# Kernel tuning notes

Measured on AMD Instinct MI355X. Metric: run time of the kernel, lower is better.

## Reference

```python
import jax, jax.numpy as jnp
import numpy as np

B, C, H, W = 16, 512, 64, 64
NH, HD = 8, 64  # num_heads, head_dim; C == NH*HD
EPS_ATTN = 1e-5
EPS_BN = 1e-5


def setup_inputs() -> dict:
    key = jax.random.key(0)
    k = jax.random.split(key, 9)
    x = jax.random.normal(k[0], (B, C, H, W), dtype=jnp.float32)
    # grouped 1x1 conv qkv: groups=NH, in/group=HD, out/group=3*HD
    w1 = jax.random.normal(k[1], (NH, 3 * HD, HD), dtype=jnp.float32) * 0.05
    b1 = jax.random.normal(k[2], (NH, 3 * HD), dtype=jnp.float32) * 0.01
    # grouped 1x1 conv qkv2: groups=HD, in/group=NH, out/group=3*NH
    w2 = jax.random.normal(k[3], (HD, 3 * NH, NH), dtype=jnp.float32) * 0.05
    b2 = jax.random.normal(k[4], (HD, 3 * NH), dtype=jnp.float32) * 0.01
    gamma = 1.0 + 0.1 * jax.random.normal(k[5], (C,), dtype=jnp.float32)
    beta = 0.1 * jax.random.normal(k[6], (C,), dtype=jnp.float32)
    rmean = 0.1 * jax.random.normal(k[7], (C,), dtype=jnp.float32)
    rvar = 0.5 + jax.random.uniform(k[8], (C,), dtype=jnp.float32)
    return {"x": x, "w1": w1, "b1": b1, "w2": w2, "b2": b2,
            "gamma": gamma, "beta": beta, "rmean": rmean, "rvar": rvar}


def _signed_sqrt_softmax(a):
    a = jnp.sign(a) * jnp.sqrt(jnp.abs(a) + EPS_ATTN)
    return jax.nn.softmax(a, axis=-1)


def reference(x, w1, b1, w2, b2, gamma, beta, rmean, rvar):
    N = H * W
    # ---- stage 1: grouped 1x1 conv (groups=NH) ----
    xg = x.reshape(B, NH, HD, N)
    qkv = jnp.einsum('goi,bgin->bgon', w1, xg) + b1[None, :, :, None]  # [B,NH,3HD,N]
    # torch grouped-conv channel order is group-major -> flatten then split as in source
    q, k, v = jnp.moveaxis(qkv.reshape(B, 3 * C, N).reshape(B, 3, NH, HD, N), 1, 0)
    attn = jnp.einsum('bhdn,bhen->bhde', q, k) * (HD ** -0.5)  # [B,NH,HD,HD]
    attn = _signed_sqrt_softmax(attn)
    out = jnp.einsum('bhde,bhen->bhdn', attn, v)  # [B,NH,HD,N]
    x1 = out.reshape(B, C, H, W) + x
    x1 = jnp.transpose(x1.reshape(B, NH, HD, H, W), (0, 2, 1, 3, 4)).reshape(B, C, H, W)
    # ---- BatchNorm2d (eval mode) + ReLU ----
    inv = gamma / jnp.sqrt(rvar + EPS_BN)
    y = x1 * inv[None, :, None, None] + (beta - rmean * inv)[None, :, None, None]
    xr = jnp.maximum(y, 0.0)
    # ---- stage 2: grouped 1x1 conv (groups=HD) ----
    xg2 = xr.reshape(B, HD, NH, N)
    qkv2 = jnp.einsum('goi,bgin->bgon', w2, xg2) + b2[None, :, :, None]  # [B,HD,3NH,N]
    q2, k2, v2 = jnp.moveaxis(qkv2.reshape(B, 3 * C, N).reshape(B, 3, HD, NH, N), 1, 0)
    attn2 = jnp.einsum('bdhn,bden->bdhe', q2, k2) * (NH ** -0.5)  # [B,HD,NH,NH]
    attn2 = _signed_sqrt_softmax(attn2)
    out2 = jnp.einsum('bdhe,bden->bdhn', attn2, v2)  # [B,HD,NH,N]
    x2 = jnp.transpose(out2.reshape(B, HD, NH, H, W), (0, 2, 1, 3, 4)).reshape(B, C, H, W) + y
    return x2
```

## Files before the change

kernel.cpp:

```cpp
#include <hip/hip_runtime.h>

#define N_ 4096

typedef __attribute__((ext_vector_type(8))) short bf16x8;
typedef __attribute__((ext_vector_type(4))) short bf16x4;
typedef __attribute__((ext_vector_type(4))) float f32x4;

__device__ __forceinline__ float ssqrt(float a) {
  if (a == 0.f) return 0.f;
  return copysignf(sqrtf(fabsf(a) + 1e-5f), a);
}

__device__ __forceinline__ ushort f2bf(float f) {
  uint u = __float_as_uint(f);
  u += 0x7fff + ((u >> 16) & 1);
  return (ushort)(u >> 16);
}
__device__ __forceinline__ float bf2f(ushort h) {
  return __uint_as_float((uint)h << 16);
}

__device__ __forceinline__ void split2(float f, ushort& hi, ushort& lo) {
  uint u = __float_as_uint(f);
  hi = (ushort)(u >> 16);
  float lof = f - __uint_as_float(u & 0xffff0000u);
  lo = (ushort)(__float_as_uint(lof) >> 16);
}

__device__ __forceinline__ f32x4 mfma16(bf16x8 a, bf16x8 b, f32x4 c) {
  return __builtin_amdgcn_mfma_f32_16x16x32_bf16(a, b, c, 0, 0, 0);
}

__device__ __forceinline__ bf16x8 relu8(bf16x8 v) {
  union { bf16x8 h; uint u[4]; } x;
  x.h = v;
#pragma unroll
  for (int i = 0; i < 4; ++i) {
    uint m = x.u[i] & 0x80008000u;
    x.u[i] &= ~((m >> 15) * 0xFFFFu);
  }
  return x.h;
}

__device__ __forceinline__ bf16x8 ld8_b64(const ushort* p) {
  bf16x4 a = *(const bf16x4*)p;
  bf16x4 b = *(const bf16x4*)(p + 4);
  return (bf16x8){a[0], a[1], a[2], a[3], b[0], b[1], b[2], b[3]};
}

__global__ __launch_bounds__(256) void k1_gram(const float* __restrict__ x,
    float* __restrict__ Gp, float* __restrict__ sums) {
  const int GQ[6] = {0, 0, 1, 1, 2, 2};
  const int GK[6] = {2, 3, 3, 4, 4, 5};
  int bid = (blockIdx.x & 7) * 48 + (blockIdx.x >> 3);
  int s = bid / 96, rem = bid % 96;
  int b = rem / 6, pid = rem % 6;
  int gq = GQ[pid], gk = GK[pid];
  const float* A = x + ((size_t)b * 512 + gq * 64) * N_ + s * 1024;
  const float* B = x + ((size_t)b * 512 + gk * 64) * N_ + s * 1024;
  __shared__ __attribute__((aligned(16))) ushort Ah[64][72], Al[64][72];
  __shared__ __attribute__((aligned(16))) ushort Bh[64][72], Bl[64][72];
  int t = threadIdx.x;
  int lr = t >> 2, lq = t & 3;
  int l = t & 63, w = t >> 6;
  int mw = (w >> 1) * 32, nw = (w & 1) * 32;
  int fr = l & 15, ko = (l >> 4) * 8;
  float sumA = 0.f, sumB = 0.f;
  f32x4 acc[2][2];
#pragma unroll
  for (int i = 0; i < 2; ++i)
#pragma unroll
    for (int j = 0; j < 2; ++j) acc[i][j] = (f32x4){0.f, 0.f, 0.f, 0.f};

  for (int kt = 0; kt < 16; ++kt) {
    int kbase = kt * 64 + lq * 16;
#pragma unroll
    for (int j = 0; j < 4; ++j) {
      float4 va = *(const float4*)(A + (size_t)lr * N_ + kbase + j * 4);
      float4 vb = *(const float4*)(B + (size_t)lr * N_ + kbase + j * 4);
      sumA += va.x + va.y + va.z + va.w;
      sumB += vb.x + vb.y + vb.z + vb.w;
      ushort4 ha, la, hb, lb;
      split2(va.x, ha.x, la.x); split2(va.y, ha.y, la.y);
      split2(va.z, ha.z, la.z); split2(va.w, ha.w, la.w);
      split2(vb.x, hb.x, lb.x); split2(vb.y, hb.y, lb.y);
      split2(vb.z, hb.z, lb.z); split2(vb.w, hb.w, lb.w);
      int c0 = lq * 16 + j * 4;
      *(ushort4*)&Ah[lr][c0] = ha;
      *(ushort4*)&Al[lr][c0] = la;
      *(ushort4*)&Bh[lr][c0] = hb;
      *(ushort4*)&Bl[lr][c0] = lb;
    }
    __syncthreads();
#pragma unroll
    for (int wk = 0; wk < 2; ++wk) {
      int kk = wk * 32 + ko;
      bf16x8 ah[2], al[2], bh[2], bl[2];
#pragma unroll
      for (int mt = 0; mt < 2; ++mt) {
        ah[mt] = *(const bf16x8*)&Ah[mw + mt * 16 + fr][kk];
        al[mt] = *(const bf16x8*)&Al[mw + mt * 16 + fr][kk];
      }
#pragma unroll
      for (int nt = 0; nt < 2; ++nt) {
        bh[nt] = *(const bf16x8*)&Bh[nw + nt * 16 + fr][kk];
        bl[nt] = *(const bf16x8*)&Bl[nw + nt * 16 + fr][kk];
      }
#pragma unroll
      for (int mt = 0; mt < 2; ++mt)
#pragma unroll
        for (int nt = 0; nt < 2; ++nt) {
          acc[mt][nt] = mfma16(ah[mt], bh[nt], acc[mt][nt]);
          acc[mt][nt] = mfma16(ah[mt], bl[nt], acc[mt][nt]);
          acc[mt][nt] = mfma16(al[mt], bh[nt], acc[mt][nt]);
        }
    }
    __syncthreads();
  }
  size_t base = ((size_t)s * 96 + rem) * 4096;
#pragma unroll
  for (int mt = 0; mt < 2; ++mt)
#pragma unroll
    for (int nt = 0; nt < 2; ++nt)
#pragma unroll
      for (int reg = 0; reg < 4; ++reg) {
        int gr = mw + mt * 16 + (l >> 4) * 4 + reg;
        int gc = nw + nt * 16 + fr;
        Gp[base + (size_t)gr * 64 + gc] = acc[mt][nt][reg];
      }
  sumA += __shfl_xor(sumA, 1); sumA += __shfl_xor(sumA, 2);
  sumB += __shfl_xor(sumB, 1); sumB += __shfl_xor(sumB, 2);
  if (lq == 0) {
    sums[(((size_t)s * 16 + b) * 6 + gq) * 64 + lr] = sumA;
    sums[(((size_t)s * 16 + b) * 6 + gk) * 64 + lr] = sumB;
  }
}

__global__ __launch_bounds__(256) void k2_attn1(
    const float* __restrict__ w1, const float* __restrict__ b1,
    const float* __restrict__ Gp, const float* __restrict__ sums,
    ushort* __restrict__ M1h, ushort* __restrict__ M1l,
    float* __restrict__ pbv1) {
  const int PID[8] = {0, 1, 1, 2, 3, 3, 4, 5};
  int bh = blockIdx.x;
  int b = bh >> 3, h = bh & 7;
  int pid = PID[h];
  int mq = h, mk = 8 + h, mv = 16 + h;
  int gq = mq / 3, oq0 = (mq % 3) * 64;
  int gk = mk / 3, ok0 = (mk % 3) * 64;
  int gv = mv / 3, ov0 = (mv % 3) * 64;
  __shared__ __attribute__((aligned(16))) float Gs[64][68];
  __shared__ __attribute__((aligned(16))) float Was[64][68];
  __shared__ __attribute__((aligned(16))) float Wbs[64][68];
  __shared__ __attribute__((aligned(16))) float Ts[64][68];
  __shared__ float sxs[64], sks[64], vqs[64], vks[64], bvs[64];
  int t = threadIdx.x, tx = t & 15, ty = t >> 4;
  int d0 = ty * 4, e0 = tx * 4;

  for (int f = t; f < 4096; f += 256) {
    int dd = f >> 6, ee = f & 63;
    float g = 0.f;
#pragma unroll
    for (int s = 0; s < 4; ++s)
      g += Gp[((size_t)s * 96 + b * 6 + pid) * 4096 + f];
    Gs[dd][ee] = g;
    Was[dd][ee] = w1[((size_t)(gq * 192 + oq0 + dd)) * 64 + ee];
    Wbs[dd][ee] = w1[((size_t)(gk * 192 + ok0 + dd)) * 64 + ee];
  }
  if (t < 64) {
    float v = 0.f, w = 0.f;
#pragma unroll
    for (int s = 0; s < 4; ++s) {
      v += sums[(((size_t)s * 16 + b) * 6 + gq) * 64 + t];
      w += sums[(((size_t)s * 16 + b) * 6 + gk) * 64 + t];
    }
    sxs[t] = v; sks[t] = w;
    bvs[t] = b1[gv * 192 + ov0 + t];
  }
  __syncthreads();
  if (t < 64) {
    float vq = 0.f, vk = 0.f;
    for (int i = 0; i < 64; ++i) { vq += Was[t][i] * sxs[i]; vk += Wbs[t][i] * sks[i]; }
    vqs[t] = vq; vks[t] = vk;
  }
  {
    float acc[4][4] = {};
    for (int i = 0; i < 64; i += 4) {
      float4 a4[4], g4[4];
#pragma unroll
      for (int r = 0; r < 4; ++r) a4[r] = *(const float4*)&Was[d0 + r][i];
#pragma unroll
      for (int k = 0; k < 4; ++k) g4[k] = *(const float4*)&Gs[i + k][e0];
#pragma unroll
      for (int r = 0; r < 4; ++r) {
        const float* ap = (const float*)&a4[r];
#pragma unroll
        for (int k = 0; k < 4; ++k) {
          const float* gp = (const float*)&g4[k];
#pragma unroll
          for (int c = 0; c < 4; ++c) acc[r][c] += ap[k] * gp[c];
        }
      }
    }
#pragma unroll
    for (int r = 0; r < 4; ++r)
#pragma unroll
      for (int c = 0; c < 4; ++c) Ts[d0 + r][e0 + c] = acc[r][c];
  }
  __syncthreads();
  float P[4][4];
  {
    float s[4][4] = {};
    for (int j = 0; j < 64; j += 4) {
      float4 t4[4], w4[4];
#pragma unroll
      for (int r = 0; r < 4; ++r) t4[r] = *(const float4*)&Ts[d0 + r][j];
#pragma unroll
      for (int c = 0; c < 4; ++c) w4[c] = *(const float4*)&Wbs[e0 + c][j];
#pragma unroll
      for (int r = 0; r < 4; ++r)
#pragma unroll
        for (int c = 0; c < 4; ++c)
          s[r][c] += t4[r].x * w4[c].x + t4[r].y * w4[c].y
                   + t4[r].z * w4[c].z + t4[r].w * w4[c].w;
    }
    float bq_[4], bk_[4];
#pragma unroll
    for (int r = 0; r < 4; ++r) bq_[r] = b1[gq * 192 + oq0 + d0 + r];
#pragma unroll
    for (int c = 0; c < 4; ++c) bk_[c] = b1[gk * 192 + ok0 + e0 + c];
#pragma unroll
    for (int r = 0; r < 4; ++r)
#pragma unroll
      for (int c = 0; c < 4; ++c) {
        float v = (s[r][c] + bq_[r] * vks[e0 + c] + bk_[c] * vqs[d0 + r]
                   + 4096.f * bq_[r] * bk_[c]) * 0.125f;
        s[r][c] = ssqrt(v);
      }
#pragma unroll
    for (int r = 0; r < 4; ++r) {
      float m = fmaxf(fmaxf(s[r][0], s[r][1]), fmaxf(s[r][2], s[r][3]));
#pragma unroll
      for (int mm = 1; mm < 16; mm <<= 1) m = fmaxf(m, __shfl_xor(m, mm));
      float sum = 0.f;
#pragma unroll
      for (int c = 0; c < 4; ++c) { s[r][c] = expf(s[r][c] - m); sum += s[r][c]; }
#pragma unroll
      for (int mm = 1; mm < 16; mm <<= 1) sum += __shfl_xor(sum, mm);
      float inv = 1.f / sum;
#pragma unroll
      for (int c = 0; c < 4; ++c) P[r][c] = s[r][c] * inv;
    }
  }
#pragma unroll
  for (int r = 0; r < 4; ++r)
#pragma unroll
    for (int c = 0; c < 4; ++c) Gs[d0 + r][e0 + c] = P[r][c];
  for (int f = t; f < 4096; f += 256) {
    int ee = f >> 6, ii = f & 63;
    Was[ee][ii] = w1[((size_t)(gv * 192 + ov0 + ee)) * 64 + ii];
  }
  __syncthreads();
  {
    float acc[4][4] = {};
    for (int e = 0; e < 64; e += 4) {
      float4 p4[4], v4[4];
#pragma unroll
      for (int r = 0; r < 4; ++r) p4[r] = *(const float4*)&Gs[d0 + r][e];
#pragma unroll
      for (int k = 0; k < 4; ++k) v4[k] = *(const float4*)&Was[e + k][e0];
#pragma unroll
      for (int r = 0; r < 4; ++r) {
        const float* pp = (const float*)&p4[r];
#pragma unroll
        for (int k = 0; k < 4; ++k) {
          const float* vp = (const float*)&v4[k];
#pragma unroll
          for (int c = 0; c < 4; ++c) acc[r][c] += pp[k] * vp[c];
        }
      }
    }
    ushort* MoH = M1h + (size_t)bh * 4096;
    ushort* MoL = M1l + (size_t)bh * 4096;
#pragma unroll
    for (int r = 0; r < 4; ++r)
#pragma unroll
      for (int c = 0; c < 4; ++c) {
        float vv = acc[r][c];
        ushort hi = f2bf(vv);
        MoH[(size_t)(d0 + r) * 64 + e0 + c] = hi;
        MoL[(size_t)(d0 + r) * 64 + e0 + c] = f2bf(vv - bf2f(hi));
      }
  }
  if (t < 64) {
    float pb = 0.f;
    for (int e = 0; e < 64; ++e) pb += Gs[t][e] * bvs[e];
    pbv1[(size_t)bh * 64 + t] = pb;
  }
}

__global__ __launch_bounds__(256) void k3_out1(const float* __restrict__ x,
    const ushort* __restrict__ M1h, const ushort* __restrict__ M1l,
    const float* __restrict__ pbv1,
    const float* __restrict__ gamma, const float* __restrict__ beta,
    const float* __restrict__ rmean, const float* __restrict__ rvar,
    ushort* __restrict__ y) {
  int orig = (blockIdx.x & 7) * 256 + (blockIdx.x >> 3);
  int b = orig >> 7;
  int rem = orig & 127;
  int chunk = rem >> 3, h = rem & 7;
  int bh = b * 8 + h;
  int gv = (16 + h) / 3;
  const float* Xv = x + ((size_t)b * 512 + gv * 64) * N_ + chunk * 256;
  const float* Xr = x + ((size_t)b * 512 + h * 64) * N_ + chunk * 256;
  ushort* Y = y + (size_t)b * 512 * N_ + chunk * 256;

  __shared__ __attribute__((aligned(16))) ushort Xth[64][68], Xtl[64][68];
  __shared__ float pbs[64], invs[64], adds[64];
  int t = threadIdx.x;
  if (t < 64) {
    pbs[t] = pbv1[(size_t)bh * 64 + t];
    int c = t * 8 + h;
    float iv = gamma[c] / sqrtf(rvar[c] + 1e-5f);
    invs[t] = iv;
    adds[t] = beta[c] - rmean[c] * iv;
  }
  int l = t & 63, w = t >> 6;
  int dq = w >> 1, nq = w & 1;
  int fr = l & 15, g = l >> 4;

  bf16x8 mh[2][2], ml[2][2];
  {
    const ushort* MbH = M1h + (size_t)bh * 4096;
    const ushort* MbL = M1l + (size_t)bh * 4096;
#pragma unroll
    for (int dr = 0; dr < 2; ++dr)
#pragma unroll
      for (int wk = 0; wk < 2; ++wk) {
        int off = (dq * 32 + dr * 16 + fr) * 64 + wk * 32 + g * 8;
        mh[dr][wk] = *(const bf16x8*)(MbH + off);
        ml[dr][wk] = *(const bf16x8*)(MbL + off);
      }
  }

  int e2 = t >> 3, q = t & 7;
  for (int tile = 0; tile < 4; ++tile) {
    int nb = tile * 64;
    {
      const float* r0p = Xv + (size_t)(2 * e2) * N_ + nb + q * 8;
      const float* r1p = r0p + N_;
      float4 a0 = *(const float4*)r0p, a1 = *(const float4*)(r0p + 4);
      float4 b0 = *(const float4*)r1p, b1 = *(const float4*)(r1p + 4);
      float ra[8] = {a0.x, a0.y, a0.z, a0.w, a1.x, a1.y, a1.z, a1.w};
      float rb[8] = {b0.x, b0.y, b0.z, b0.w, b1.x, b1.y, b1.z, b1.w};
#pragma unroll
      for (int i = 0; i < 8; ++i) {
        int n = q * 8 + i;
        ushort h0, l0, h1, l1;
        split2(ra[i], h0, l0);
        split2(rb[i], h1, l1);
        *(uint*)&Xth[n][2 * e2] = (uint)h0 | ((uint)h1 << 16);
        *(uint*)&Xtl[n][2 * e2] = (uint)l0 | ((uint)l1 << 16);
      }
    }
    __syncthreads();
    f32x4 acc[2][2];
#pragma unroll
    for (int i = 0; i < 2; ++i)
#pragma unroll
      for (int j = 0; j < 2; ++j) acc[i][j] = (f32x4){0.f, 0.f, 0.f, 0.f};
#pragma unroll
    for (int wk = 0; wk < 2; ++wk) {
      int kk = wk * 32 + g * 8;
      bf16x8 xh[2], xl[2];
#pragma unroll
      for (int nr = 0; nr < 2; ++nr) {
        xh[nr] = ld8_b64(&Xth[nq * 32 + nr * 16 + fr][kk]);
        xl[nr] = ld8_b64(&Xtl[nq * 32 + nr * 16 + fr][kk]);
      }
#pragma unroll
      for (int nr = 0; nr < 2; ++nr)
#pragma unroll
        for (int dr = 0; dr < 2; ++dr) {
          acc[nr][dr] = mfma16(xh[nr], mh[dr][wk], acc[nr][dr]);
          acc[nr][dr] = mfma16(xh[nr], ml[dr][wk], acc[nr][dr]);
          acc[nr][dr] = mfma16(xl[nr], mh[dr][wk], acc[nr][dr]);
        }
    }
#pragma unroll
    for (int nr = 0; nr < 2; ++nr)
#pragma unroll
      for (int dr = 0; dr < 2; ++dr) {
        int d = dq * 32 + dr * 16 + fr;
        int n0 = nb + nq * 32 + nr * 16 + g * 4;
        float4 rx = *(const float4*)(Xr + (size_t)d * N_ + n0);
        float iv = invs[d], ad = adds[d], pb = pbs[d];
        float4 v;
        v.x = (acc[nr][dr][0] + pb + rx.x) * iv + ad;
        v.y = (acc[nr][dr][1] + pb + rx.y) * iv + ad;
        v.z = (acc[nr][dr][2] + pb + rx.z) * iv + ad;
        v.w = (acc[nr][dr][3] + pb + rx.w) * iv + ad;
        ushort4 o;
        o.x = f2bf(v.x); o.y = f2bf(v.y); o.z = f2bf(v.z); o.w = f2bf(v.w);
        *(ushort4*)(Y + (size_t)(d * 8 + h) * N_ + n0) = o;
      }
    __syncthreads();
  }
}

__global__ __launch_bounds__(256) void k46_stage2(const ushort* __restrict__ y,
    const float* __restrict__ w2, const float* __restrict__ b2,
    float* __restrict__ out) {
  int orig = (blockIdx.x & 7) * 128 + (blockIdx.x >> 3);
  int b = orig >> 6, d = orig & 63;
  int gq = d / 3, gk = (64 + d) / 3, gv = (128 + d) / 3;
  int mq = d, mk = 64 + d, mv = 128 + d;
  int g2q = mq / 3, oq0 = (mq % 3) * 8;
  int g2k = mk / 3, ok0 = (mk % 3) * 8;
  int g2v = mv / 3, ov0 = (mv % 3) * 8;
  const ushort* Aq = y + ((size_t)b * 512 + gq * 8) * N_;
  const ushort* Ak = y + ((size_t)b * 512 + gk * 8) * N_;
  int t = threadIdx.x;
  int l = t & 63, w = t >> 6;

  __shared__ float W2q[8][8], W2k[8][8], W2v[8][8];
  __shared__ float bq2[8], bk2[8], bv2[8];
  __shared__ float red[4][16][16];
  __shared__ float gbuf[80];
  __shared__ float Ps[8][9];
  __shared__ float Msh[8][8], pbsh[8];
  if (t < 64) {
    int hh = t >> 3, ee = t & 7;
    W2q[hh][ee] = w2[(size_t)(g2q * 24 + oq0 + hh) * 8 + ee];
    W2k[hh][ee] = w2[(size_t)(g2k * 24 + ok0 + hh) * 8 + ee];
    W2v[hh][ee] = w2[(size_t)(g2v * 24 + ov0 + hh) * 8 + ee];
  }
  if (t < 8) {
    bq2[t] = b2[g2q * 24 + oq0 + t];
    bk2[t] = b2[g2k * 24 + ok0 + t];
    bv2[t] = b2[g2v * 24 + ov0 + t];
  }

  {
    int row16 = l & 15;
    int ko = (l >> 4) * 8;
    const ushort* Arow = (row16 < 8) ? (Aq + (size_t)row16 * N_)
                                     : (Ak + (size_t)(row16 - 8) * N_);
    const ushort* Brow = (row16 < 8) ? (Ak + (size_t)row16 * N_) : nullptr;
    ushort bv = (row16 == 8) ? (ushort)0x3F80 : (ushort)0;
    bf16x8 bconst = {(short)bv, (short)bv, (short)bv, (short)bv,
                     (short)bv, (short)bv, (short)bv, (short)bv};
    f32x4 acc = (f32x4){0.f, 0.f, 0.f, 0.f};
    int nbase = w * 1024 + ko;
#pragma unroll 4
    for (int step = 0; step < 32; ++step) {
      int n0 = nbase + step * 32;
      bf16x8 a = relu8(*(const bf16x8*)(Arow + n0));
      bf16x8 bb;
      if (row16 < 8) bb = relu8(*(const bf16x8*)(Brow + n0));
      else bb = bconst;
      acc = mfma16(a, bb, acc);
    }
#pragma unroll
    for (int r = 0; r < 4; ++r) red[w][(l >> 4) * 4 + r][l & 15] = acc[r];
  }
  __syncthreads();
  {
    int rr = t >> 4, cc = t & 15;
    float csum = red[0][rr][cc] + red[1][rr][cc] + red[2][rr][cc] + red[3][rr][cc];
    if (rr < 8 && cc < 8) gbuf[rr * 8 + cc] = csum;
    else if (cc == 8) gbuf[rr < 8 ? 64 + rr : 72 + (rr - 8)] = csum;
  }
  __syncthreads();

  if (t < 64) {
    int hh = t >> 3, ee = t & 7;
    float s = 0.f;
#pragma unroll
    for (int i = 0; i < 8; ++i) {
      float pg = 0.f;
#pragma unroll
      for (int j = 0; j < 8; ++j) pg += gbuf[i * 8 + j] * W2k[ee][j];
      s += W2q[hh][i] * pg;
    }
    float dq = 0.f, dk = 0.f;
#pragma unroll
    for (int i = 0; i < 8; ++i) { dq += W2q[hh][i] * gbuf[64 + i]; dk += W2k[ee][i] * gbuf[72 + i]; }
    s = (s + bq2[hh] * dk + bk2[ee] * dq + 4096.f * bq2[hh] * bk2[ee]) * 0.35355339059327373f;
    s = ssqrt(s);
    float m = s;
#pragma unroll
    for (int mm = 1; mm < 8; mm <<= 1) m = fmaxf(m, __shfl_xor(m, mm));
    float p = expf(s - m);
    float sum = p;
#pragma unroll
    for (int mm = 1; mm < 8; mm <<= 1) sum += __shfl_xor(sum, mm);
    p /= sum;
    Ps[hh][ee] = p;
  }
  __syncthreads();
  if (t < 64) {
    int hh = t >> 3, ee = t & 7;
    float mo = 0.f;
#pragma unroll
    for (int e = 0; e < 8; ++e) mo += Ps[hh][e] * W2v[e][ee];
    Msh[hh][ee] = mo;
  }
  if (t < 8) {
    float pb = 0.f;
#pragma unroll
    for (int e = 0; e < 8; ++e) pb += Ps[t][e] * bv2[e];
    pbsh[t] = pb;
  }
  __syncthreads();

  float msr[8][8], pbr[8];
#pragma unroll
  for (int hh = 0; hh < 8; ++hh) {
    pbr[hh] = pbsh[hh];
#pragma unroll
    for (int i = 0; i < 8; ++i) msr[hh][i] = Msh[hh][i];
  }
  const ushort* Yv = y + ((size_t)b * 512 + gv * 8) * N_;
  const ushort* Yr = y + ((size_t)b * 512 + d) * N_;
  float* O = out + ((size_t)b * 512 + d) * N_;
  for (int it = 0; it < 4; ++it) {
    int n4 = (it * 256 + t) * 4;
    float xv0[8], xv1[8], xv2[8], xv3[8];
#pragma unroll
    for (int i = 0; i < 8; ++i) {
      ushort4 u = *(const ushort4*)(Yv + (size_t)i * N_ + n4);
      xv0[i] = fmaxf(bf2f(u.x), 0.f); xv1[i] = fmaxf(bf2f(u.y), 0.f);
      xv2[i] = fmaxf(bf2f(u.z), 0.f); xv3[i] = fmaxf(bf2f(u.w), 0.f);
    }
#pragma unroll
    for (int hh = 0; hh < 8; ++hh) {
      float4 a;
      a.x = pbr[hh]; a.y = pbr[hh]; a.z = pbr[hh]; a.w = pbr[hh];
#pragma unroll
      for (int i = 0; i < 8; ++i) {
        float m = msr[hh][i];
        a.x += m * xv0[i]; a.y += m * xv1[i];
        a.z += m * xv2[i]; a.w += m * xv3[i];
      }
      ushort4 r = *(const ushort4*)(Yr + (size_t)hh * 64 * N_ + n4);
      a.x += bf2f(r.x); a.y += bf2f(r.y); a.z += bf2f(r.z); a.w += bf2f(r.w);
      *(float4*)(O + (size_t)hh * 64 * N_ + n4) = a;
    }
  }
}

extern "C" void kernel_launch(void* const* d_in, const int* in_sizes, int n_in,
                              void* d_out, int out_size, void* d_ws, size_t ws_size,
                              hipStream_t stream) {
  const float* x     = (const float*)d_in[0];
  const float* w1    = (const float*)d_in[1];
  const float* b1    = (const float*)d_in[2];
  const float* w2    = (const float*)d_in[3];
  const float* b2    = (const float*)d_in[4];
  const float* gamma = (const float*)d_in[5];
  const float* beta  = (const float*)d_in[6];
  const float* rmean = (const float*)d_in[7];
  const float* rvar  = (const float*)d_in[8];
  float* out = (float*)d_out;

  ushort* y    = (ushort*)d_ws;
  float* Gp    = (float*)(y + 33554432);
  float* sums  = Gp + 1572864;
  ushort* M1h  = (ushort*)(sums + 24576);
  ushort* M1l  = M1h + 524288;
  float* pbv1  = (float*)(M1l + 524288);
  size_t need = (size_t)67108864 + 6291456 + 98304 + 2097152 + 32768;
  if (ws_size < need) return;

  k1_gram<<<384, 256, 0, stream>>>(x, Gp, sums);
  k2_attn1<<<128, 256, 0, stream>>>(w1, b1, Gp, sums, M1h, M1l, pbv1);
  k3_out1<<<2048, 256, 0, stream>>>(x, M1h, M1l, pbv1, gamma, beta, rmean, rvar, y);
  k46_stage2<<<1024, 256, 0, stream>>>(y, w2, b2, out);
}
```

Baseline: 169.2 us.

## Split stage-2 kernel into separate Gram and output kernels with 4x grid

Splits the fused stage-2 kernel into two. The first computes partial Gram sums over four N-chunks and writes them to a workspace buffer. The second sums those partials, computes the softmax, and applies the output transform on one chunk per block. Each kernel launches 4096 blocks instead of 1024, which raises parallelism and shortens the serial Gram phase inside each block. In exchange it adds a kernel launch, a small workspace round trip, and redundant per-block softmax and weight setup across the four chunks.

```diff
diff --git a/kernel.cpp b/kernel.cpp
--- a/kernel.cpp
+++ b/kernel.cpp
@@ -408,24 +408,66 @@
   }
 }
 
-__global__ __launch_bounds__(256) void k46_stage2(const ushort* __restrict__ y,
+__global__ __launch_bounds__(256) void k4a_gram2(const ushort* __restrict__ y,
+    float* __restrict__ Gpart) {
+  int orig = (blockIdx.x & 7) * 512 + (blockIdx.x >> 3);
+  int bd = orig >> 2, chunk = orig & 3;
+  int b = bd >> 6, d = bd & 63;
+  int gq = d / 3, gk = (64 + d) / 3;
+  const ushort* Aq = y + ((size_t)b * 512 + gq * 8) * N_;
+  const ushort* Ak = y + ((size_t)b * 512 + gk * 8) * N_;
+  int t = threadIdx.x;
+  int l = t & 63, w = t >> 6;
+  __shared__ float red[4][16][16];
+
+  int row16 = l & 15;
+  int ko = (l >> 4) * 8;
+  const ushort* Arow = (row16 < 8) ? (Aq + (size_t)row16 * N_)
+                                   : (Ak + (size_t)(row16 - 8) * N_);
+  const ushort* Brow = (row16 < 8) ? (Ak + (size_t)row16 * N_) : nullptr;
+  ushort bv = (row16 == 8) ? (ushort)0x3F80 : (ushort)0;
+  bf16x8 bconst = {(short)bv, (short)bv, (short)bv, (short)bv,
+                   (short)bv, (short)bv, (short)bv, (short)bv};
+  f32x4 acc = (f32x4){0.f, 0.f, 0.f, 0.f};
+  int nbase = chunk * 1024 + w * 256 + ko;
+#pragma unroll
+  for (int step = 0; step < 8; ++step) {
+    int n0 = nbase + step * 32;
+    bf16x8 a = relu8(*(const bf16x8*)(Arow + n0));
+    bf16x8 bb;
+    if (row16 < 8) bb = relu8(*(const bf16x8*)(Brow + n0));
+    else bb = bconst;
+    acc = mfma16(a, bb, acc);
+  }
+#pragma unroll
+  for (int r = 0; r < 4; ++r) red[w][(l >> 4) * 4 + r][l & 15] = acc[r];
+  __syncthreads();
+  {
+    int rr = t >> 4, cc = t & 15;
+    float csum = red[0][rr][cc] + red[1][rr][cc] + red[2][rr][cc] + red[3][rr][cc];
+    int idx = -1;
+    if (rr < 8 && cc < 8) idx = rr * 8 + cc;
+    else if (cc == 8) idx = (rr < 8) ? 64 + rr : 72 + (rr - 8);
+    if (idx >= 0) Gpart[((size_t)bd * 4 + chunk) * 80 + idx] = csum;
+  }
+}
+
+__global__ __launch_bounds__(256) void k6_pv(const ushort* __restrict__ y,
+    const float* __restrict__ Gpart,
     const float* __restrict__ w2, const float* __restrict__ b2,
     float* __restrict__ out) {
-  int orig = (blockIdx.x & 7) * 128 + (blockIdx.x >> 3);
-  int b = orig >> 6, d = orig & 63;
-  int gq = d / 3, gk = (64 + d) / 3, gv = (128 + d) / 3;
+  int orig = (blockIdx.x & 7) * 512 + (blockIdx.x >> 3);
+  int bd = orig >> 2, chunk = orig & 3;
+  int b = bd >> 6, d = bd & 63;
+  int gv = (128 + d) / 3;
   int mq = d, mk = 64 + d, mv = 128 + d;
   int g2q = mq / 3, oq0 = (mq % 3) * 8;
   int g2k = mk / 3, ok0 = (mk % 3) * 8;
   int g2v = mv / 3, ov0 = (mv % 3) * 8;
-  const ushort* Aq = y + ((size_t)b * 512 + gq * 8) * N_;
-  const ushort* Ak = y + ((size_t)b * 512 + gk * 8) * N_;
   int t = threadIdx.x;
-  int l = t & 63, w = t >> 6;
 
   __shared__ float W2q[8][8], W2k[8][8], W2v[8][8];
   __shared__ float bq2[8], bk2[8], bv2[8];
-  __shared__ float red[4][16][16];
   __shared__ float gbuf[80];
   __shared__ float Ps[8][9];
   __shared__ float Msh[8][8], pbsh[8];
@@ -440,36 +482,11 @@
     bk2[t] = b2[g2k * 24 + ok0 + t];
     bv2[t] = b2[g2v * 24 + ov0 + t];
   }
-
-  {
-    int row16 = l & 15;
-    int ko = (l >> 4) * 8;
-    const ushort* Arow = (row16 < 8) ? (Aq + (size_t)row16 * N_)
-                                     : (Ak + (size_t)(row16 - 8) * N_);
-    const ushort* Brow = (row16 < 8) ? (Ak + (size_t)row16 * N_) : nullptr;
-    ushort bv = (row16 == 8) ? (ushort)0x3F80 : (ushort)0;
-    bf16x8 bconst = {(short)bv, (short)bv, (short)bv, (short)bv,
-                     (short)bv, (short)bv, (short)bv, (short)bv};
-    f32x4 acc = (f32x4){0.f, 0.f, 0.f, 0.f};
-    int nbase = w * 1024 + ko;
-#pragma unroll 4
-    for (int step = 0; step < 32; ++step) {
-      int n0 = nbase + step * 32;
-      bf16x8 a = relu8(*(const bf16x8*)(Arow + n0));
-      bf16x8 bb;
-      if (row16 < 8) bb = relu8(*(const bf16x8*)(Brow + n0));
-      else bb = bconst;
-      acc = mfma16(a, bb, acc);
-    }
-#pragma unroll
-    for (int r = 0; r < 4; ++r) red[w][(l >> 4) * 4 + r][l & 15] = acc[r];
-  }
-  __syncthreads();
-  {
-    int rr = t >> 4, cc = t & 15;
-    float csum = red[0][rr][cc] + red[1][rr][cc] + red[2][rr][cc] + red[3][rr][cc];
-    if (rr < 8 && cc < 8) gbuf[rr * 8 + cc] = csum;
-    else if (cc == 8) gbuf[rr < 8 ? 64 + rr : 72 + (rr - 8)] = csum;
+  if (t < 80) {
+    float g = 0.f;
+#pragma unroll
+    for (int c = 0; c < 4; ++c) g += Gpart[((size_t)bd * 4 + c) * 80 + t];
+    gbuf[t] = g;
   }
   __syncthreads();
 
@@ -496,7 +513,7 @@
 #pragma unroll
     for (int mm = 1; mm < 8; mm <<= 1) sum += __shfl_xor(sum, mm);
     p /= sum;
-    Ps[hh][ee] = p;
+    Ps[t >> 3][t & 7] = p;
   }
   __syncthreads();
   if (t < 64) {
@@ -524,29 +541,27 @@
   const ushort* Yv = y + ((size_t)b * 512 + gv * 8) * N_;
   const ushort* Yr = y + ((size_t)b * 512 + d) * N_;
   float* O = out + ((size_t)b * 512 + d) * N_;
-  for (int it = 0; it < 4; ++it) {
-    int n4 = (it * 256 + t) * 4;
-    float xv0[8], xv1[8], xv2[8], xv3[8];
+  int n4 = chunk * 1024 + t * 4;
+  float xv0[8], xv1[8], xv2[8], xv3[8];
+#pragma unroll
+  for (int i = 0; i < 8; ++i) {
+    ushort4 u = *(const ushort4*)(Yv + (size_t)i * N_ + n4);
+    xv0[i] = fmaxf(bf2f(u.x), 0.f); xv1[i] = fmaxf(bf2f(u.y), 0.f);
+    xv2[i] = fmaxf(bf2f(u.z), 0.f); xv3[i] = fmaxf(bf2f(u.w), 0.f);
+  }
+#pragma unroll
+  for (int hh = 0; hh < 8; ++hh) {
+    float4 a;
+    a.x = pbr[hh]; a.y = pbr[hh]; a.z = pbr[hh]; a.w = pbr[hh];
 #pragma unroll
     for (int i = 0; i < 8; ++i) {
-      ushort4 u = *(const ushort4*)(Yv + (size_t)i * N_ + n4);
-      xv0[i] = fmaxf(bf2f(u.x), 0.f); xv1[i] = fmaxf(bf2f(u.y), 0.f);
-      xv2[i] = fmaxf(bf2f(u.z), 0.f); xv3[i] = fmaxf(bf2f(u.w), 0.f);
-    }
-#pragma unroll
-    for (int hh = 0; hh < 8; ++hh) {
-      float4 a;
-      a.x = pbr[hh]; a.y = pbr[hh]; a.z = pbr[hh]; a.w = pbr[hh];
-#pragma unroll
-      for (int i = 0; i < 8; ++i) {
-        float m = msr[hh][i];
-        a.x += m * xv0[i]; a.y += m * xv1[i];
-        a.z += m * xv2[i]; a.w += m * xv3[i];
-      }
-      ushort4 r = *(const ushort4*)(Yr + (size_t)hh * 64 * N_ + n4);
-      a.x += bf2f(r.x); a.y += bf2f(r.y); a.z += bf2f(r.z); a.w += bf2f(r.w);
-      *(float4*)(O + (size_t)hh * 64 * N_ + n4) = a;
-    }
+      float m = msr[hh][i];
+      a.x += m * xv0[i]; a.y += m * xv1[i];
+      a.z += m * xv2[i]; a.w += m * xv3[i];
+    }
+    ushort4 r = *(const ushort4*)(Yr + (size_t)hh * 64 * N_ + n4);
+    a.x += bf2f(r.x); a.y += bf2f(r.y); a.z += bf2f(r.z); a.w += bf2f(r.w);
+    *(float4*)(O + (size_t)hh * 64 * N_ + n4) = a;
   }
 }
 
@@ -570,11 +585,13 @@
   ushort* M1h  = (ushort*)(sums + 24576);
   ushort* M1l  = M1h + 524288;
   float* pbv1  = (float*)(M1l + 524288);
-  size_t need = (size_t)67108864 + 6291456 + 98304 + 2097152 + 32768;
+  float* Gpart = pbv1 + 8192;
+  size_t need = (size_t)67108864 + 6291456 + 98304 + 2097152 + 32768 + 1310720;
   if (ws_size < need) return;
 
   k1_gram<<<384, 256, 0, stream>>>(x, Gp, sums);
   k2_attn1<<<128, 256, 0, stream>>>(w1, b1, Gp, sums, M1h, M1l, pbv1);
   k3_out1<<<2048, 256, 0, stream>>>(x, M1h, M1l, pbv1, gamma, beta, rmean, rvar, y);
-  k46_stage2<<<1024, 256, 0, stream>>>(y, w2, b2, out);
-}
+  k4a_gram2<<<4096, 256, 0, stream>>>(y, Gpart);
+  k6_pv<<<4096, 256, 0, stream>>>(y, Gpart, w2, b2, out);
+}
```

After: 178.1 us. 5.3% more time.
